# Kernel optimization log

Hardware: AMD Instinct MI355X
Metric: run time of the kernel (lower is better)

The kernel has to match this reference:

```python
import jax, jax.numpy as jnp
import numpy as np

EMBED_DIM = 1024
NUM_HEADS = 16
HEAD_DIM = EMBED_DIM // NUM_HEADS


def setup_inputs() -> dict:
    key = jax.random.key(0)
    ks = jax.random.split(key, 12)
    B, S, D = 4, 2048, EMBED_DIM
    scale = 1.0 / np.sqrt(D)
    inp = {
        "query": jax.random.normal(ks[0], (B, S, D), jnp.float32),
        "key": jax.random.normal(ks[1], (B, S, D), jnp.float32),
        "value": jax.random.normal(ks[2], (B, S, D), jnp.float32),
        # nn.Linear weights: [out_features, in_features], y = x @ W.T + b
        "Wq": jax.random.normal(ks[3], (D, D), jnp.float32) * scale,
        "bq": jnp.zeros((D,), jnp.float32),
        "Wk": jax.random.normal(ks[4], (D, D), jnp.float32) * scale,
        "bk": jnp.zeros((D,), jnp.float32),
        "Wv": jax.random.normal(ks[5], (D, D), jnp.float32) * scale,
        "bv": jnp.zeros((D,), jnp.float32),
        "Wo": jax.random.normal(ks[6], (D, D), jnp.float32) * scale,
        "bo": jnp.zeros((D,), jnp.float32),
    }
    return inp


def reference(query, key, value, Wq, bq, Wk, bk, Wv, bv, Wo, bo):
    B, Sq, D = query.shape
    Sk = key.shape[1]
    H, Dh = NUM_HEADS, HEAD_DIM

    def proj(x, W, b):
        # [B,S,D] -> [B,H,S,Dh]
        y = jnp.einsum('bsd,ed->bse', x, W) + b
        return y.reshape(x.shape[0], x.shape[1], H, Dh).transpose(0, 2, 1, 3)

    q = proj(query, Wq, bq)
    k = proj(key, Wk, bk)
    v = proj(value, Wv, bv)

    # sigmoid attention (no softmax); dropout is identity in eval mode
    scores = jnp.einsum('bhqd,bhkd->bhqk', q, k) / jnp.sqrt(jnp.float32(Dh)).astype(q.dtype)
    attn = jax.nn.sigmoid(scores)
    out = jnp.einsum('bhqk,bhkd->bhqd', attn, v)

    out = out.transpose(0, 2, 1, 3).reshape(B, Sq, D)
    return jnp.einsum('bsd,ed->bse', out, Wo) + bo
```

## Files before the change

### kernel.cpp

```cpp
#include <hip/hip_runtime.h>


typedef _Float16 f16x2 __attribute__((ext_vector_type(2)));
typedef _Float16 f16x4 __attribute__((ext_vector_type(4)));
typedef _Float16 f16x8 __attribute__((ext_vector_type(8)));
typedef __fp16   h16x2 __attribute__((ext_vector_type(2)));
typedef float    f32x4 __attribute__((ext_vector_type(4)));
typedef float    f32x16 __attribute__((ext_vector_type(16)));

typedef __attribute__((address_space(3))) void* lds_vp;
typedef const __attribute__((address_space(1))) void* gbl_vp;

__device__ __forceinline__ void gld_lds16(const void* g, void* l) {
  __builtin_amdgcn_global_load_lds((gbl_vp)g, (lds_vp)l, 16, 0, 0);
}

__device__ __forceinline__ f16x8 cvt8(float4 a, float4 b) {
  return (f16x8){(_Float16)a.x, (_Float16)a.y, (_Float16)a.z, (_Float16)a.w,
                 (_Float16)b.x, (_Float16)b.y, (_Float16)b.z, (_Float16)b.w};
}

__device__ __forceinline__ f16x2 pk2(float a, float b) {
  h16x2 r = __builtin_amdgcn_cvt_pkrtz(a, b);
  return __builtin_bit_cast(f16x2, r);
}

__device__ __forceinline__ float exp2_fast(float x) {
#if __has_builtin(__builtin_amdgcn_exp2f)
  return __builtin_amdgcn_exp2f(x);
#else
  float r;
  asm("v_exp_f32 %0, %1" : "=v"(r) : "v"(x));
  return r;
#endif
}

#define BM 128
#define BN 128
#define BK 32

template <bool AF16, bool BF16, bool TRANSV, bool OUTF32>
__global__ __launch_bounds__(256) void gemm_bt(const void* __restrict__ Av,
                                               const void* __restrict__ Bv,
                                               const float* __restrict__ bias,
                                               void* __restrict__ Yv,
                                               int M, int N, int K) {
  __shared__ __align__(16) _Float16 sA[BM * BK];
  __shared__ __align__(16) _Float16 sB[BN * BK];

  const int t = threadIdx.x, lane = t & 63, wid = t >> 6;
  const int m0 = blockIdx.x * BM, n0 = blockIdx.y * BN;
  const int wm = (wid >> 1) * 64, wn = (wid & 1) * 64;
  const int lrow = lane & 15, g = lane >> 4;

  f32x4 acc[4][4] = {};

  const int arow = 16 * wid + (lane >> 2);
  const int gq = (lane & 3) ^ ((lane >> 3) & 3);
  _Float16* lA1 = sA + wid * 512;
  _Float16* lA2 = sA + 2048 + wid * 512;
  _Float16* lB1 = sB + wid * 512;
  _Float16* lB2 = sB + 2048 + wid * 512;

  const int mrow = t >> 1, mhalf = t & 1;
  const int mm = (mrow >> 1) & 3;
  const int ch_lo = mrow * 4 + ((2 * mhalf) ^ mm);
  const int ch_hi = ch_lo ^ 1;

  const _Float16* pA16a = nullptr; const _Float16* pA16b = nullptr;
  const float* pA32 = nullptr;
  if constexpr (AF16) {
    const _Float16* A = (const _Float16*)Av;
    pA16a = A + (size_t)(m0 + arow) * K + gq * 8;
    pA16b = A + (size_t)(m0 + 64 + arow) * K + gq * 8;
  } else {
    pA32 = (const float*)Av + (size_t)(m0 + mrow) * K + mhalf * 16;
  }
  const _Float16* pB16a = nullptr; const _Float16* pB16b = nullptr;
  const float* pB32 = nullptr;
  if constexpr (BF16) {
    const _Float16* B = (const _Float16*)Bv;
    pB16a = B + (size_t)(n0 + arow) * K + gq * 8;
    pB16b = B + (size_t)(n0 + 64 + arow) * K + gq * 8;
  } else {
    pB32 = (const float*)Bv + (size_t)(n0 + mrow) * K + mhalf * 16;
  }

  const int xr = g ^ ((lrow >> 1) & 3);

  for (int k0 = 0; k0 < K; k0 += BK) {
    float4 av[4], bv4[4];
    if constexpr (!AF16) {
      const float4* p = (const float4*)(pA32 + k0);
      av[0] = p[0]; av[1] = p[1]; av[2] = p[2]; av[3] = p[3];
    }
    if constexpr (!BF16) {
      const float4* p = (const float4*)(pB32 + k0);
      bv4[0] = p[0]; bv4[1] = p[1]; bv4[2] = p[2]; bv4[3] = p[3];
    }
    __syncthreads();
    if constexpr (AF16) {
      gld_lds16(pA16a + k0, lA1);
      gld_lds16(pA16b + k0, lA2);
    } else {
      *(f16x8*)(sA + ch_lo * 8) = cvt8(av[0], av[1]);
      *(f16x8*)(sA + ch_hi * 8) = cvt8(av[2], av[3]);
    }
    if constexpr (BF16) {
      gld_lds16(pB16a + k0, lB1);
      gld_lds16(pB16b + k0, lB2);
    } else {
      *(f16x8*)(sB + ch_lo * 8) = cvt8(bv4[0], bv4[1]);
      *(f16x8*)(sB + ch_hi * 8) = cvt8(bv4[2], bv4[3]);
    }
    __syncthreads();

    f16x8 af[4], bf[4];
#pragma unroll
    for (int i = 0; i < 4; i++)
      af[i] = *(const f16x8*)(sA + (wm + i * 16 + lrow) * 32 + xr * 8);
#pragma unroll
    for (int j = 0; j < 4; j++)
      bf[j] = *(const f16x8*)(sB + (wn + j * 16 + lrow) * 32 + xr * 8);
#pragma unroll
    for (int i = 0; i < 4; i++)
#pragma unroll
      for (int j = 0; j < 4; j++)
        acc[i][j] = __builtin_amdgcn_mfma_f32_16x16x32_f16(af[i], bf[j], acc[i][j], 0, 0, 0);
  }

  const int orow = g * 4, ocol = lrow;
#pragma unroll
  for (int j = 0; j < 4; j++) {
    const int col = n0 + wn + j * 16 + ocol;
    const float bv = bias[col];
#pragma unroll
    for (int i = 0; i < 4; i++) {
      const int row = m0 + wm + i * 16 + orow;
      if constexpr (TRANSV) {
        _Float16* VT = (_Float16*)Yv;
        int s = row & 2047;
        int sp = (s & ~12) | ((s & 4) << 1) | ((s & 8) >> 1);
        _Float16* dst = VT + (((size_t)(row >> 11) * 16 + (col >> 6)) * 64 + (col & 63)) * 2048 + sp;
        f16x4 v = {(_Float16)(acc[i][j][0] + bv), (_Float16)(acc[i][j][1] + bv),
                   (_Float16)(acc[i][j][2] + bv), (_Float16)(acc[i][j][3] + bv)};
        *(f16x4*)dst = v;
      } else if constexpr (OUTF32) {
        float* Y = (float*)Yv;
#pragma unroll
        for (int r = 0; r < 4; r++) Y[(size_t)(row + r) * N + col] = acc[i][j][r] + bv;
      } else {
        _Float16* Y = (_Float16*)Yv;
#pragma unroll
        for (int r = 0; r < 4; r++) Y[(size_t)(row + r) * N + col] = (_Float16)(acc[i][j][r] + bv);
      }
    }
  }
}

__global__ __launch_bounds__(256) void qkv_gemm(const _Float16* __restrict__ Xq,
                                                const _Float16* __restrict__ Xk,
                                                const _Float16* __restrict__ Xv,
                                                const _Float16* __restrict__ W,
                                                const float* __restrict__ bq,
                                                const float* __restrict__ bk,
                                                const float* __restrict__ bv,
                                                _Float16* __restrict__ Qo,
                                                _Float16* __restrict__ Ko,
                                                _Float16* __restrict__ VT) {
  __shared__ __align__(16) _Float16 sA[BM * BK];
  __shared__ __align__(16) _Float16 sB[BN * BK];

  const int t = threadIdx.x, lane = t & 63, wid = t >> 6;
  const int n0g = blockIdx.x * BN, m0 = blockIdx.y * BM;
  const int seg = blockIdx.x >> 3, n0 = n0g & 1023;
  const _Float16* A = (seg == 0) ? Xq : (seg == 1) ? Xk : Xv;
  const float* bias = (seg == 0) ? bq : (seg == 1) ? bk : bv;
  const int K = 1024;

  const int wm = (wid >> 1) * 64, wn = (wid & 1) * 64;
  const int lrow = lane & 15, g = lane >> 4;

  f32x4 acc[4][4] = {};

  const int arow = 16 * wid + (lane >> 2);
  const int gq = (lane & 3) ^ ((lane >> 3) & 3);
  _Float16* lA1 = sA + wid * 512;
  _Float16* lA2 = sA + 2048 + wid * 512;
  _Float16* lB1 = sB + wid * 512;
  _Float16* lB2 = sB + 2048 + wid * 512;

  const _Float16* pA16a = A + (size_t)(m0 + arow) * K + gq * 8;
  const _Float16* pA16b = A + (size_t)(m0 + 64 + arow) * K + gq * 8;
  const _Float16* pB16a = W + (size_t)(n0g + arow) * K + gq * 8;
  const _Float16* pB16b = W + (size_t)(n0g + 64 + arow) * K + gq * 8;

  const int xr = g ^ ((lrow >> 1) & 3);

  for (int k0 = 0; k0 < K; k0 += BK) {
    __syncthreads();
    gld_lds16(pA16a + k0, lA1);
    gld_lds16(pA16b + k0, lA2);
    gld_lds16(pB16a + k0, lB1);
    gld_lds16(pB16b + k0, lB2);
    __syncthreads();

    f16x8 af[4], bf[4];
#pragma unroll
    for (int i = 0; i < 4; i++)
      af[i] = *(const f16x8*)(sA + (wm + i * 16 + lrow) * 32 + xr * 8);
#pragma unroll
    for (int j = 0; j < 4; j++)
      bf[j] = *(const f16x8*)(sB + (wn + j * 16 + lrow) * 32 + xr * 8);
#pragma unroll
    for (int i = 0; i < 4; i++)
#pragma unroll
      for (int j = 0; j < 4; j++)
        acc[i][j] = __builtin_amdgcn_mfma_f32_16x16x32_f16(af[i], bf[j], acc[i][j], 0, 0, 0);
  }

  const int orow = g * 4, ocol = lrow;
#pragma unroll
  for (int j = 0; j < 4; j++) {
    const int col = n0 + wn + j * 16 + ocol;
    const float bvv = bias[col];
#pragma unroll
    for (int i = 0; i < 4; i++) {
      const int row = m0 + wm + i * 16 + orow;
      if (seg == 2) {
        int s = row & 2047;
        int sp = (s & ~12) | ((s & 4) << 1) | ((s & 8) >> 1);
        _Float16* dst = VT + (((size_t)(row >> 11) * 16 + (col >> 6)) * 64 + (col & 63)) * 2048 + sp;
        f16x4 v = {(_Float16)(acc[i][j][0] + bvv), (_Float16)(acc[i][j][1] + bvv),
                   (_Float16)(acc[i][j][2] + bvv), (_Float16)(acc[i][j][3] + bvv)};
        *(f16x4*)dst = v;
      } else {
        _Float16* Y = (seg == 0) ? Qo : Ko;
#pragma unroll
        for (int r = 0; r < 4; r++) Y[(size_t)(row + r) * 1024 + col] = (_Float16)(acc[i][j][r] + bvv);
      }
    }
  }
}

#define LDS_ROW 72
#define TILE_E (64 * LDS_ROW)

__global__ __launch_bounds__(256, 2) void attn_sig(const _Float16* __restrict__ Q,
                                                   const _Float16* __restrict__ K,
                                                   const _Float16* __restrict__ VT,
                                                   _Float16* __restrict__ O) {
  __shared__ __align__(16) _Float16 smem[4 * TILE_E];

  const int t = threadIdx.x, lane = t & 63, wid = t >> 6;
  const int l31 = lane & 31, g5 = lane >> 5;
  const int li = (int)(blockIdx.x + 8 * blockIdx.y + 128 * blockIdx.z);
  const int swz = (li & 7) * 64 + (li >> 3);
  const int qb = swz & 7, hb = swz >> 3;
  const int h = hb & 15, b = hb >> 4;
  const int q0 = qb * 256;
  const int qw = q0 + wid * 64;
  const int NT = 32;

  f16x8 qf0[4], qf1[4];
  {
    const _Float16* qp = Q + (size_t)(b * 2048 + qw + l31) * 1024 + h * 64;
#pragma unroll
    for (int dhc = 0; dhc < 4; dhc++) {
      qf0[dhc] = *(const f16x8*)(qp + dhc * 16 + g5 * 8) * (_Float16)-0.18033688f;
      qf1[dhc] = *(const f16x8*)(qp + 32 * 1024 + dhc * 16 + g5 * 8) * (_Float16)-0.18033688f;
    }
  }

  f32x16 oacc00 = {}, oacc01 = {}, oacc10 = {}, oacc11 = {};

  const int srow = t >> 2, scol = (t & 3) * 16;
  const _Float16* kbase = K + ((size_t)(b * 2048) + srow) * 1024 + h * 64 + scol;
  const _Float16* vbase = VT + ((size_t)((b * 16 + h) * 64 + srow)) * 2048 + scol;

#define LOAD_TILE(tile)                                                  \
  ka = *(const uint4*)(kbase + (size_t)(tile) * 64 * 1024);              \
  kb = *(const uint4*)(kbase + (size_t)(tile) * 64 * 1024 + 8);          \
  va = *(const uint4*)(vbase + (tile) * 64);                             \
  vb = *(const uint4*)(vbase + (tile) * 64 + 8);

#define WRITE_TILE(p)                                                    \
  {                                                                      \
    _Float16* dK = smem + (p) * 2 * TILE_E;                              \
    _Float16* dV = dK + TILE_E;                                          \
    *(uint4*)&dK[srow * LDS_ROW + scol] = ka;                            \
    *(uint4*)&dK[srow * LDS_ROW + scol + 8] = kb;                        \
    *(uint4*)&dV[srow * LDS_ROW + scol] = va;                            \
    *(uint4*)&dV[srow * LDS_ROW + scol + 8] = vb;                        \
  }

#define PACK_PF(pf, sacc)                                                \
  {                                                                      \
    _Pragma("unroll")                                                    \
    for (int G = 0; G < 2; G++) {                                        \
      union { f16x8 v; f16x2 hh[4]; } u;                                 \
      _Pragma("unroll")                                                  \
      for (int pr = 0; pr < 4; pr++) {                                   \
        float e0 = exp2_fast(sacc[G * 8 + pr * 2 + 0]);                  \
        float e1 = exp2_fast(sacc[G * 8 + pr * 2 + 1]);                  \
        u.hh[pr] = pk2(__builtin_amdgcn_rcpf(1.0f + e0),                 \
                       __builtin_amdgcn_rcpf(1.0f + e1));                \
      }                                                                  \
      pf[G] = u.v;                                                       \
    }                                                                    \
  }

#define CHUNK(c)                                                                      \
  {                                                                                   \
    const _Float16* sk_ = sKp + ((c) * 32 + l31) * LDS_ROW + g5 * 8;                  \
    f16x8 kf0 = *(const f16x8*)(sk_ + 0);                                             \
    f16x8 kf1 = *(const f16x8*)(sk_ + 16);                                            \
    f16x8 kf2 = *(const f16x8*)(sk_ + 32);                                            \
    f16x8 kf3 = *(const f16x8*)(sk_ + 48);                                            \
    f32x16 s0 = {}, s1 = {};                                                          \
    __builtin_amdgcn_s_setprio(1);                                                    \
    s0 = __builtin_amdgcn_mfma_f32_32x32x16_f16(kf0, qf0[0], s0, 0, 0, 0);            \
    s1 = __builtin_amdgcn_mfma_f32_32x32x16_f16(kf0, qf1[0], s1, 0, 0, 0);            \
    s0 = __builtin_amdgcn_mfma_f32_32x32x16_f16(kf1, qf0[1], s0, 0, 0, 0);            \
    s1 = __builtin_amdgcn_mfma_f32_32x32x16_f16(kf1, qf1[1], s1, 0, 0, 0);            \
    s0 = __builtin_amdgcn_mfma_f32_32x32x16_f16(kf2, qf0[2], s0, 0, 0, 0);            \
    s1 = __builtin_amdgcn_mfma_f32_32x32x16_f16(kf2, qf1[2], s1, 0, 0, 0);            \
    s0 = __builtin_amdgcn_mfma_f32_32x32x16_f16(kf3, qf0[3], s0, 0, 0, 0);            \
    s1 = __builtin_amdgcn_mfma_f32_32x32x16_f16(kf3, qf1[3], s1, 0, 0, 0);            \
    __builtin_amdgcn_s_setprio(0);                                                    \
    f16x8 pf0[2], pf1[2];                                                             \
    PACK_PF(pf0, s0);                                                                 \
    PACK_PF(pf1, s1);                                                                 \
    const _Float16* sv_ = sVp + l31 * LDS_ROW + (c) * 32 + g5 * 8;                    \
    f16x8 vf00 = *(const f16x8*)(sv_ + 0);                                            \
    f16x8 vf01 = *(const f16x8*)(sv_ + 16);                                           \
    f16x8 vf10 = *(const f16x8*)(sv_ + 32 * LDS_ROW);                                 \
    f16x8 vf11 = *(const f16x8*)(sv_ + 32 * LDS_ROW + 16);                            \
    __builtin_amdgcn_s_setprio(1);                                                    \
    oacc00 = __builtin_amdgcn_mfma_f32_32x32x16_f16(vf00, pf0[0], oacc00, 0, 0, 0);   \
    oacc10 = __builtin_amdgcn_mfma_f32_32x32x16_f16(vf00, pf1[0], oacc10, 0, 0, 0);   \
    oacc01 = __builtin_amdgcn_mfma_f32_32x32x16_f16(vf10, pf0[0], oacc01, 0, 0, 0);   \
    oacc11 = __builtin_amdgcn_mfma_f32_32x32x16_f16(vf10, pf1[0], oacc11, 0, 0, 0);   \
    oacc00 = __builtin_amdgcn_mfma_f32_32x32x16_f16(vf01, pf0[1], oacc00, 0, 0, 0);   \
    oacc10 = __builtin_amdgcn_mfma_f32_32x32x16_f16(vf01, pf1[1], oacc10, 0, 0, 0);   \
    oacc01 = __builtin_amdgcn_mfma_f32_32x32x16_f16(vf11, pf0[1], oacc01, 0, 0, 0);   \
    oacc11 = __builtin_amdgcn_mfma_f32_32x32x16_f16(vf11, pf1[1], oacc11, 0, 0, 0);   \
    __builtin_amdgcn_s_setprio(0);                                                    \
  }

  uint4 ka, kb, va, vb;

  LOAD_TILE(0);
  WRITE_TILE(0);
  LOAD_TILE(1);

  for (int tt = 0; tt < NT; ++tt) {
    const int p = tt & 1;
    const _Float16* sKp = smem + p * 2 * TILE_E;
    const _Float16* sVp = sKp + TILE_E;
    __syncthreads();
    if (tt + 1 < NT) { WRITE_TILE(p ^ 1); }
    if (tt + 2 < NT) { LOAD_TILE(tt + 2); }
    CHUNK(0);
    CHUNK(1);
  }

  _Float16* ep = smem;
#pragma unroll
  for (int pass = 0; pass < 2; pass++) {
    __syncthreads();
    if ((wid >> 1) == pass) {
      const int rbase = (wid & 1) * 64;
#pragma unroll
      for (int c = 0; c < 4; c++) {
        f16x4 a0 = {(_Float16)oacc00[4 * c + 0], (_Float16)oacc00[4 * c + 1],
                    (_Float16)oacc00[4 * c + 2], (_Float16)oacc00[4 * c + 3]};
        f16x4 a1 = {(_Float16)oacc01[4 * c + 0], (_Float16)oacc01[4 * c + 1],
                    (_Float16)oacc01[4 * c + 2], (_Float16)oacc01[4 * c + 3]};
        *(f16x4*)&ep[(rbase + l31) * LDS_ROW + 0 * 32 + c * 8 + g5 * 4] = a0;
        *(f16x4*)&ep[(rbase + l31) * LDS_ROW + 1 * 32 + c * 8 + g5 * 4] = a1;
        f16x4 b0 = {(_Float16)oacc10[4 * c + 0], (_Float16)oacc10[4 * c + 1],
                    (_Float16)oacc10[4 * c + 2], (_Float16)oacc10[4 * c + 3]};
        f16x4 b1 = {(_Float16)oacc11[4 * c + 0], (_Float16)oacc11[4 * c + 1],
                    (_Float16)oacc11[4 * c + 2], (_Float16)oacc11[4 * c + 3]};
        *(f16x4*)&ep[(rbase + 32 + l31) * LDS_ROW + 0 * 32 + c * 8 + g5 * 4] = b0;
        *(f16x4*)&ep[(rbase + 32 + l31) * LDS_ROW + 1 * 32 + c * 8 + g5 * 4] = b1;
      }
    }
    __syncthreads();
#pragma unroll
    for (int i = 0; i < 4; i++) {
      const int q = i * 32 + (t >> 3), dhc = t & 7;
      f16x8 row = *(const f16x8*)&ep[q * LDS_ROW + dhc * 8];
      *(f16x8*)(O + (size_t)(b * 2048 + q0 + pass * 128 + q) * 1024 + h * 64 + dhc * 8) = row;
    }
  }
#undef LOAD_TILE
#undef WRITE_TILE
#undef PACK_PF
#undef CHUNK
}

struct CvtArgs {
  const float* src[7];
  _Float16* dst[7];
  int n[7];
  int cnt;
};

__global__ __launch_bounds__(256) void cvt_f32_f16(CvtArgs a) {
  const int ti = blockIdx.y;
  if (ti >= a.cnt) return;
  const int i = (blockIdx.x * 256 + threadIdx.x) * 8;
  if (i >= a.n[ti]) return;
  const float4* s = (const float4*)(a.src[ti] + i);
  float4 x = s[0], y = s[1];
  *(f16x8*)(a.dst[ti] + i) = cvt8(x, y);
}

extern "C" void kernel_launch(void* const* d_in, const int* in_sizes, int n_in,
                              void* d_out, int out_size, void* d_ws, size_t ws_size,
                              hipStream_t stream) {
  const float* query = (const float*)d_in[0];
  const float* key   = (const float*)d_in[1];
  const float* value = (const float*)d_in[2];
  const float* Wq = (const float*)d_in[3];
  const float* bq = (const float*)d_in[4];
  const float* Wk = (const float*)d_in[5];
  const float* bk = (const float*)d_in[6];
  const float* Wv = (const float*)d_in[7];
  const float* bv = (const float*)d_in[8];
  const float* Wo = (const float*)d_in[9];
  const float* bo = (const float*)d_in[10];
  float* out = (float*)d_out;

  const int D = 1024, M = 8192;
  const size_t MB = 1024 * 1024;
  char* ws = (char*)d_ws;
  dim3 bb(256);

  if (ws_size >= 104 * MB) {
    _Float16* Xq = (_Float16*)(ws + 0 * MB);
    _Float16* Xk = (_Float16*)(ws + 16 * MB);
    _Float16* Xv = (_Float16*)(ws + 32 * MB);
    _Float16* Qp = (_Float16*)(ws + 48 * MB);
    _Float16* Kp = (_Float16*)(ws + 64 * MB);
    _Float16* VT = (_Float16*)(ws + 80 * MB);
    _Float16* Wf = (_Float16*)(ws + 96 * MB);
    _Float16* AO = Xq;
    CvtArgs ca{};
    ca.src[0] = query; ca.dst[0] = Xq; ca.n[0] = M * D;
    ca.src[1] = key;   ca.dst[1] = Xk; ca.n[1] = M * D;
    ca.src[2] = value; ca.dst[2] = Xv; ca.n[2] = M * D;
    ca.src[3] = Wq; ca.dst[3] = Wf + 0 * 1048576; ca.n[3] = D * D;
    ca.src[4] = Wk; ca.dst[4] = Wf + 1 * 1048576; ca.n[4] = D * D;
    ca.src[5] = Wv; ca.dst[5] = Wf + 2 * 1048576; ca.n[5] = D * D;
    ca.src[6] = Wo; ca.dst[6] = Wf + 3 * 1048576; ca.n[6] = D * D;
    ca.cnt = 7;
    cvt_f32_f16<<<dim3(4096, 7), bb, 0, stream>>>(ca);
    qkv_gemm<<<dim3(24, 64), bb, 0, stream>>>(Xq, Xk, Xv, Wf, bq, bk, bv, Qp, Kp, VT);
    attn_sig<<<dim3(8, 16, 4), bb, 0, stream>>>(Qp, Kp, VT, AO);
    gemm_bt<true, true, false, true><<<dim3(64, 8), bb, 0, stream>>>(AO, Wf + 3 * 1048576, bo, out, M, D, D);
  } else {
    _Float16* Qp = (_Float16*)(ws + 0 * MB);
    _Float16* Kp = (_Float16*)(ws + 16 * MB);
    _Float16* VT = (_Float16*)(ws + 32 * MB);
    _Float16* AO = (_Float16*)(ws + 48 * MB);
    gemm_bt<false, false, false, false><<<dim3(64, 8), bb, 0, stream>>>(query, Wq, bq, Qp, M, D, D);
    gemm_bt<false, false, false, false><<<dim3(64, 8), bb, 0, stream>>>(key,   Wk, bk, Kp, M, D, D);
    gemm_bt<false, false, true,  false><<<dim3(64, 8), bb, 0, stream>>>(value, Wv, bv, VT, M, D, D);
    attn_sig<<<dim3(8, 16, 4), bb, 0, stream>>>(Qp, Kp, VT, AO);
    gemm_bt<true, false, false, true><<<dim3(64, 8), bb, 0, stream>>>(AO, Wo, bo, out, M, D, D);
  }
}
```

Baseline: 354.2 us.

## Split attention key range across two blocks and sum partial outputs

The sigmoid attention kernel now splits the key sequence into two halves, one per block. This doubles the grid to 1024 one-dimensional blocks, each with half as many key tiles. Each half writes its fp16 partial output to its own buffer, and a new add_halves kernel sums the two. This works because sigmoid attention has no softmax normalization to combine. The launch bound is raised to 4 blocks per CU to increase occupancy, at the risk of register pressure or spills, extra partial-output memory traffic, one more launch, and fp16 rounding of the partials.

```diff
diff --git a/kernel.cpp b/kernel.cpp
--- a/kernel.cpp
+++ b/kernel.cpp
@@ -246,7 +246,7 @@
 #define LDS_ROW 72
 #define TILE_E (64 * LDS_ROW)
 
-__global__ __launch_bounds__(256, 2) void attn_sig(const _Float16* __restrict__ Q,
+__global__ __launch_bounds__(256, 4) void attn_sig(const _Float16* __restrict__ Q,
                                                    const _Float16* __restrict__ K,
                                                    const _Float16* __restrict__ VT,
                                                    _Float16* __restrict__ O) {
@@ -254,13 +254,13 @@
 
   const int t = threadIdx.x, lane = t & 63, wid = t >> 6;
   const int l31 = lane & 31, g5 = lane >> 5;
-  const int li = (int)(blockIdx.x + 8 * blockIdx.y + 128 * blockIdx.z);
-  const int swz = (li & 7) * 64 + (li >> 3);
-  const int qb = swz & 7, hb = swz >> 3;
-  const int h = hb & 15, b = hb >> 4;
+  const int li = (int)blockIdx.x;
+  const int swz = (li & 7) * 128 + (li >> 3);
+  const int qb = swz & 7, kh = (swz >> 3) & 1, bh = swz >> 4;
+  const int h = bh & 15, b = bh >> 4;
   const int q0 = qb * 256;
   const int qw = q0 + wid * 64;
-  const int NT = 32;
+  const int NT = 16;
 
   f16x8 qf0[4], qf1[4];
   {
@@ -275,8 +275,8 @@
   f32x16 oacc00 = {}, oacc01 = {}, oacc10 = {}, oacc11 = {};
 
   const int srow = t >> 2, scol = (t & 3) * 16;
-  const _Float16* kbase = K + ((size_t)(b * 2048) + srow) * 1024 + h * 64 + scol;
-  const _Float16* vbase = VT + ((size_t)((b * 16 + h) * 64 + srow)) * 2048 + scol;
+  const _Float16* kbase = K + ((size_t)(b * 2048) + kh * 1024 + srow) * 1024 + h * 64 + scol;
+  const _Float16* vbase = VT + ((size_t)((b * 16 + h) * 64 + srow)) * 2048 + kh * 1024 + scol;
 
 #define LOAD_TILE(tile)                                                  \
   ka = *(const uint4*)(kbase + (size_t)(tile) * 64 * 1024);              \
@@ -365,6 +365,7 @@
     CHUNK(1);
   }
 
+  _Float16* Ob = O + (size_t)kh * (8192 * 1024);
   _Float16* ep = smem;
 #pragma unroll
   for (int pass = 0; pass < 2; pass++) {
@@ -392,13 +393,23 @@
     for (int i = 0; i < 4; i++) {
       const int q = i * 32 + (t >> 3), dhc = t & 7;
       f16x8 row = *(const f16x8*)&ep[q * LDS_ROW + dhc * 8];
-      *(f16x8*)(O + (size_t)(b * 2048 + q0 + pass * 128 + q) * 1024 + h * 64 + dhc * 8) = row;
+      *(f16x8*)(Ob + (size_t)(b * 2048 + q0 + pass * 128 + q) * 1024 + h * 64 + dhc * 8) = row;
     }
   }
 #undef LOAD_TILE
 #undef WRITE_TILE
 #undef PACK_PF
 #undef CHUNK
+}
+
+__global__ __launch_bounds__(256) void add_halves(const _Float16* __restrict__ a,
+                                                  const _Float16* __restrict__ b,
+                                                  _Float16* __restrict__ o, int n) {
+  const int i = (blockIdx.x * 256 + threadIdx.x) * 8;
+  if (i >= n) return;
+  f16x8 x = *(const f16x8*)(a + i);
+  f16x8 y = *(const f16x8*)(b + i);
+  *(f16x8*)(o + i) = x + y;
 }
 
 struct CvtArgs {
@@ -447,7 +458,9 @@
     _Float16* Kp = (_Float16*)(ws + 64 * MB);
     _Float16* VT = (_Float16*)(ws + 80 * MB);
     _Float16* Wf = (_Float16*)(ws + 96 * MB);
-    _Float16* AO = Xq;
+    _Float16* AO0 = Xq;
+    _Float16* AO1 = Xk;
+    _Float16* AO  = Xv;
     CvtArgs ca{};
     ca.src[0] = query; ca.dst[0] = Xq; ca.n[0] = M * D;
     ca.src[1] = key;   ca.dst[1] = Xk; ca.n[1] = M * D;
@@ -459,17 +472,20 @@
     ca.cnt = 7;
     cvt_f32_f16<<<dim3(4096, 7), bb, 0, stream>>>(ca);
     qkv_gemm<<<dim3(24, 64), bb, 0, stream>>>(Xq, Xk, Xv, Wf, bq, bk, bv, Qp, Kp, VT);
-    attn_sig<<<dim3(8, 16, 4), bb, 0, stream>>>(Qp, Kp, VT, AO);
+    attn_sig<<<dim3(1024), bb, 0, stream>>>(Qp, Kp, VT, AO0);
+    add_halves<<<dim3(4096), bb, 0, stream>>>(AO0, AO1, AO, M * D);
     gemm_bt<true, true, false, true><<<dim3(64, 8), bb, 0, stream>>>(AO, Wf + 3 * 1048576, bo, out, M, D, D);
   } else {
     _Float16* Qp = (_Float16*)(ws + 0 * MB);
     _Float16* Kp = (_Float16*)(ws + 16 * MB);
     _Float16* VT = (_Float16*)(ws + 32 * MB);
-    _Float16* AO = (_Float16*)(ws + 48 * MB);
+    _Float16* AO0 = (_Float16*)(ws + 48 * MB);
+    _Float16* AO1 = (_Float16*)(ws + 64 * MB);
     gemm_bt<false, false, false, false><<<dim3(64, 8), bb, 0, stream>>>(query, Wq, bq, Qp, M, D, D);
     gemm_bt<false, false, false, false><<<dim3(64, 8), bb, 0, stream>>>(key,   Wk, bk, Kp, M, D, D);
     gemm_bt<false, false, true,  false><<<dim3(64, 8), bb, 0, stream>>>(value, Wv, bv, VT, M, D, D);
-    attn_sig<<<dim3(8, 16, 4), bb, 0, stream>>>(Qp, Kp, VT, AO);
-    gemm_bt<true, false, false, true><<<dim3(64, 8), bb, 0, stream>>>(AO, Wo, bo, out, M, D, D);
-  }
-}
+    attn_sig<<<dim3(1024), bb, 0, stream>>>(Qp, Kp, VT, AO0);
+    add_halves<<<dim3(4096), bb, 0, stream>>>(AO0, AO1, AO0, M * D);
+    gemm_bt<true, false, false, true><<<dim3(64, 8), bb, 0, stream>>>(AO0, Wo, bo, out, M, D, D);
+  }
+}
```

Result: slower. 715.4 us (+102.0%).

## Fuse fp32-to-fp16 activation conversion into QKV GEMM A-tile loads

Applied to the files above, without the earlier changes.

Drops the separate conversion pass over query/key/value. The QKV GEMM now reads fp32 activations directly, converts them to fp16 in registers and stores them swizzled into LDS. The conversion kernel now handles only the four weight matrices, and the workspace shrinks. This removes a full read and write of three 32MB activation tensors. In exchange, the GEMM reads twice the bytes per A tile, re-reads each activation for every N block, and uses synchronous register loads instead of direct-to-LDS loads.

```diff
diff --git a/kernel.cpp b/kernel.cpp
--- a/kernel.cpp
+++ b/kernel.cpp
@@ -158,9 +158,9 @@
   }
 }
 
-__global__ __launch_bounds__(256) void qkv_gemm(const _Float16* __restrict__ Xq,
-                                                const _Float16* __restrict__ Xk,
-                                                const _Float16* __restrict__ Xv,
+__global__ __launch_bounds__(256) void qkv_gemm(const float* __restrict__ Xq,
+                                                const float* __restrict__ Xk,
+                                                const float* __restrict__ Xv,
                                                 const _Float16* __restrict__ W,
                                                 const float* __restrict__ bq,
                                                 const float* __restrict__ bk,
@@ -174,7 +174,7 @@
   const int t = threadIdx.x, lane = t & 63, wid = t >> 6;
   const int n0g = blockIdx.x * BN, m0 = blockIdx.y * BM;
   const int seg = blockIdx.x >> 3, n0 = n0g & 1023;
-  const _Float16* A = (seg == 0) ? Xq : (seg == 1) ? Xk : Xv;
+  const float* A = (seg == 0) ? Xq : (seg == 1) ? Xk : Xv;
   const float* bias = (seg == 0) ? bq : (seg == 1) ? bk : bv;
   const int K = 1024;
 
@@ -185,22 +185,29 @@
 
   const int arow = 16 * wid + (lane >> 2);
   const int gq = (lane & 3) ^ ((lane >> 3) & 3);
-  _Float16* lA1 = sA + wid * 512;
-  _Float16* lA2 = sA + 2048 + wid * 512;
   _Float16* lB1 = sB + wid * 512;
   _Float16* lB2 = sB + 2048 + wid * 512;
 
-  const _Float16* pA16a = A + (size_t)(m0 + arow) * K + gq * 8;
-  const _Float16* pA16b = A + (size_t)(m0 + 64 + arow) * K + gq * 8;
+  const int mrow = t >> 1, mhalf = t & 1;
+  const int mm = (mrow >> 1) & 3;
+  const int ch_lo = mrow * 4 + ((2 * mhalf) ^ mm);
+  const int ch_hi = ch_lo ^ 1;
+  const float* pA32 = A + (size_t)(m0 + mrow) * K + mhalf * 16;
+
   const _Float16* pB16a = W + (size_t)(n0g + arow) * K + gq * 8;
   const _Float16* pB16b = W + (size_t)(n0g + 64 + arow) * K + gq * 8;
 
   const int xr = g ^ ((lrow >> 1) & 3);
 
   for (int k0 = 0; k0 < K; k0 += BK) {
-    __syncthreads();
-    gld_lds16(pA16a + k0, lA1);
-    gld_lds16(pA16b + k0, lA2);
+    float4 av[4];
+    {
+      const float4* p = (const float4*)(pA32 + k0);
+      av[0] = p[0]; av[1] = p[1]; av[2] = p[2]; av[3] = p[3];
+    }
+    __syncthreads();
+    *(f16x8*)(sA + ch_lo * 8) = cvt8(av[0], av[1]);
+    *(f16x8*)(sA + ch_hi * 8) = cvt8(av[2], av[3]);
     gld_lds16(pB16a + k0, lB1);
     gld_lds16(pB16b + k0, lB2);
     __syncthreads();
@@ -439,26 +446,20 @@
   char* ws = (char*)d_ws;
   dim3 bb(256);
 
-  if (ws_size >= 104 * MB) {
-    _Float16* Xq = (_Float16*)(ws + 0 * MB);
-    _Float16* Xk = (_Float16*)(ws + 16 * MB);
-    _Float16* Xv = (_Float16*)(ws + 32 * MB);
-    _Float16* Qp = (_Float16*)(ws + 48 * MB);
-    _Float16* Kp = (_Float16*)(ws + 64 * MB);
-    _Float16* VT = (_Float16*)(ws + 80 * MB);
-    _Float16* Wf = (_Float16*)(ws + 96 * MB);
-    _Float16* AO = Xq;
+  if (ws_size >= 72 * MB) {
+    _Float16* Qp = (_Float16*)(ws + 0 * MB);
+    _Float16* Kp = (_Float16*)(ws + 16 * MB);
+    _Float16* VT = (_Float16*)(ws + 32 * MB);
+    _Float16* AO = (_Float16*)(ws + 48 * MB);
+    _Float16* Wf = (_Float16*)(ws + 64 * MB);
     CvtArgs ca{};
-    ca.src[0] = query; ca.dst[0] = Xq; ca.n[0] = M * D;
-    ca.src[1] = key;   ca.dst[1] = Xk; ca.n[1] = M * D;
-    ca.src[2] = value; ca.dst[2] = Xv; ca.n[2] = M * D;
-    ca.src[3] = Wq; ca.dst[3] = Wf + 0 * 1048576; ca.n[3] = D * D;
-    ca.src[4] = Wk; ca.dst[4] = Wf + 1 * 1048576; ca.n[4] = D * D;
-    ca.src[5] = Wv; ca.dst[5] = Wf + 2 * 1048576; ca.n[5] = D * D;
-    ca.src[6] = Wo; ca.dst[6] = Wf + 3 * 1048576; ca.n[6] = D * D;
-    ca.cnt = 7;
-    cvt_f32_f16<<<dim3(4096, 7), bb, 0, stream>>>(ca);
-    qkv_gemm<<<dim3(24, 64), bb, 0, stream>>>(Xq, Xk, Xv, Wf, bq, bk, bv, Qp, Kp, VT);
+    ca.src[0] = Wq; ca.dst[0] = Wf + 0 * 1048576; ca.n[0] = D * D;
+    ca.src[1] = Wk; ca.dst[1] = Wf + 1 * 1048576; ca.n[1] = D * D;
+    ca.src[2] = Wv; ca.dst[2] = Wf + 2 * 1048576; ca.n[2] = D * D;
+    ca.src[3] = Wo; ca.dst[3] = Wf + 3 * 1048576; ca.n[3] = D * D;
+    ca.cnt = 4;
+    cvt_f32_f16<<<dim3(512, 4), bb, 0, stream>>>(ca);
+    qkv_gemm<<<dim3(24, 64), bb, 0, stream>>>(query, key, value, Wf, bq, bk, bv, Qp, Kp, VT);
     attn_sig<<<dim3(8, 16, 4), bb, 0, stream>>>(Qp, Kp, VT, AO);
     gemm_bt<true, true, false, true><<<dim3(64, 8), bb, 0, stream>>>(AO, Wf + 3 * 1048576, bo, out, M, D, D);
   } else {
```

Measured after the change: 383.1 us. +8.2%, slower.
